# Performance work log

Hardware: AMD Instinct MI355X
Metric: run time of the kernel (lower is better)

The kernel has to match this reference:

```python
import jax, jax.numpy as jnp
import numpy as np
import math

B, S, D_MODEL = 2, 2048, 1024
H = 16
DK = D_MODEL // H          # 64, down-proj per-stream dim
NOPE, ROPE = 128, 64
D_HEAD = NOPE + ROPE       # 192 = d_latent // H
D_LATENT = H * D_HEAD      # 3072
ROT_DIM = 2 * ((ROPE // 2) // 2)  # rotary dim actually rotated = qk_rope_dim//2 = 32
EPS = 1e-6


def _rmsnorm(x, w):
    out = x * jax.lax.rsqrt(jnp.mean(x * x, axis=-1, keepdims=True) + EPS)
    return out * w


def _apply_rope(x):
    # x: [b, h, s, d]; rotate first ROT_DIM channels, interleaved pairing
    s = x.shape[-2]
    inv_freq = 1.0 / (10000.0 ** (jnp.arange(0, ROT_DIM, 2, dtype=jnp.float32) / ROT_DIM))
    freqs = jnp.arange(s, dtype=jnp.float32)[:, None] * inv_freq[None, :]  # [s, ROT_DIM//2]
    freqs = jnp.repeat(freqs, 2, axis=-1)  # [s, ROT_DIM], (f0,f0,f1,f1,...)
    cos, sin = jnp.cos(freqs), jnp.sin(freqs)
    xl, xr = x[..., :ROT_DIM], x[..., ROT_DIM:]
    x1, x2 = xl[..., 0::2], xl[..., 1::2]
    rot = jnp.stack([-x2, x1], axis=-1).reshape(xl.shape)
    xl = xl * cos + rot * sin
    return jnp.concatenate([xl, xr], axis=-1)


def setup_inputs() -> dict:
    key = jax.random.key(0)
    ks = jax.random.split(key, 5)
    sc = 0.02
    x = jax.random.normal(ks[0], (B, S, D_MODEL), jnp.float32)
    mask = jnp.broadcast_to(jnp.tril(jnp.ones((S, S), jnp.int32)), (B, S, S))
    w_down = jax.random.normal(ks[1], (D_MODEL, 3 * DK), jnp.float32) * sc
    rms_w = jnp.ones((3 * DK,), jnp.float32)
    w_up = jax.random.normal(ks[2], (3 * DK, 3 * D_LATENT), jnp.float32) * sc
    w_o = jax.random.normal(ks[3], (D_LATENT, D_MODEL), jnp.float32) * sc
    return {"x": x, "mask": mask, "w_down": w_down, "rms_w": rms_w, "w_up": w_up, "w_o": w_o}


def reference(x, mask, w_down, rms_w, w_up, w_o):
    h = x @ w_down                        # [b, s, 3*dk]
    h = _rmsnorm(h, rms_w)
    qkv = h @ w_up                        # [b, s, 3*d_latent]
    q, k, v = jnp.split(qkv, 3, axis=-1)  # each [b, s, d_latent]

    def to_heads(t):
        # einops '(d h)': d outer, h inner
        return t.reshape(B, S, D_HEAD, H).transpose(0, 3, 1, 2)  # [b, h, s, d]

    q, k, v = to_heads(q), to_heads(k), to_heads(v)
    q_nope, q_rope = q[..., :NOPE], q[..., NOPE:]
    k_nope, k_rope = k[..., :NOPE], k[..., NOPE:]
    q_rope = _apply_rope(q_rope)
    k_rope = _apply_rope(k_rope)

    scores = (jnp.einsum('bhid,bhjd->bhij', q_nope, k_nope)
              + jnp.einsum('bhid,bhjd->bhij', q_rope, k_rope))
    scores = scores / math.sqrt(NOPE + ROPE)
    scores = jnp.where(mask[:, None] == 0, -1e9, scores)
    attn = jax.nn.softmax(scores, axis=-1)

    out = jnp.einsum('bhij,bhjd->bhid', attn, v)        # [b, h, s, d]
    out = out.transpose(0, 2, 1, 3).reshape(B, S, D_LATENT)  # 'b h s d -> b s (h d)'
    return out @ w_o
```

## Files before the change

### kernel.cpp

```cpp
#include <hip/hip_runtime.h>
#include <stdint.h>
#include <stddef.h>


typedef __bf16 bf16x8 __attribute__((ext_vector_type(8)));
typedef float  f32x4  __attribute__((ext_vector_type(4)));

#define MFMA16x16(a,b,c) __builtin_amdgcn_mfma_f32_16x16x32_bf16((a),(b),(c),0,0,0)

__device__ __forceinline__ uint16_t f2bf(float f){
  union { float f; uint32_t u; } v; v.f = f;
  uint32_t u = v.u + 0x7fffu + ((v.u >> 16) & 1u);
  return (uint16_t)(u >> 16);
}
__device__ __forceinline__ bf16x8 load_frag(const uint16_t* p){
  uint4 u = *reinterpret_cast<const uint4*>(p);
  return __builtin_bit_cast(bf16x8, u);
}
__device__ __forceinline__ f32x4 fzero(){
  f32x4 z = {0.f, 0.f, 0.f, 0.f};
  return z;
}
__device__ __forceinline__ uint32_t pack2(float a, float b){
  return (uint32_t)f2bf(a) | ((uint32_t)f2bf(b) << 16);
}
__device__ __forceinline__ void gl2lds16(const uint16_t* g, uint16_t* l){
  __builtin_amdgcn_global_load_lds(
      (const __attribute__((address_space(1))) uint32_t*)g,
      (__attribute__((address_space(3))) uint32_t*)l,
      16, 0, 0);
}

__global__ __launch_bounds__(256) void k_transpose_cvt(const float* __restrict__ in,
                                                       uint16_t* __restrict__ out,
                                                       int R, int C){
  __shared__ float t[32][33];
  const int tc = blockIdx.x * 32;
  const int tr = blockIdx.y * 32;
  const int j = threadIdx.x & 31, i0 = threadIdx.x >> 5;
  for(int ii = 0; ii < 4; ++ii){
    int r = i0 + ii * 8;
    t[r][j] = in[(size_t)(tr + r) * C + tc + j];
  }
  __syncthreads();
  for(int ii = 0; ii < 4; ++ii){
    int c = i0 + ii * 8;
    out[(size_t)(tc + c) * R + tr + j] = f2bf(t[j][c]);
  }
}

__global__ __launch_bounds__(256) void k_down_mfma(const float* __restrict__ x,
                                                   const uint16_t* __restrict__ wdt,
                                                   const float* __restrict__ rms_w,
                                                   uint16_t* __restrict__ h_out){
  __shared__ __align__(16) uint16_t as[32 * 64];
  __shared__ float hsq[32];
  const int tid  = threadIdx.x;
  const int wave = tid >> 6, lane = tid & 63;
  const int ml = lane & 15, qd = lane >> 4;
  const int m0 = blockIdx.x * 32;
  const int n0w = wave * 48;
  if(tid < 32) hsq[tid] = 0.f;

  f32x4 acc[2][3];
#pragma unroll
  for(int mt = 0; mt < 2; ++mt)
#pragma unroll
    for(int nt = 0; nt < 3; ++nt) acc[mt][nt] = fzero();

  const int srow = tid >> 3, sc = tid & 7;
  for(int kt = 0; kt < 16; ++kt){
    const float* src = x + (size_t)(m0 + srow) * 1024 + kt * 64 + sc * 8;
    float4 a = *reinterpret_cast<const float4*>(src);
    float4 b = *reinterpret_cast<const float4*>(src + 4);
    uint4 pk;
    pk.x = pack2(a.x, a.y); pk.y = pack2(a.z, a.w);
    pk.z = pack2(b.x, b.y); pk.w = pack2(b.z, b.w);
    __syncthreads();
    *reinterpret_cast<uint4*>(as + srow * 64 + ((sc ^ (srow & 7)) * 8)) = pk;
    __syncthreads();
#pragma unroll
    for(int kk = 0; kk < 2; ++kk){
      bf16x8 af[2];
#pragma unroll
      for(int mt = 0; mt < 2; ++mt){
        int row = mt * 16 + ml;
        af[mt] = load_frag(as + row * 64 + (((kk * 4 + qd) ^ (row & 7)) * 8));
      }
#pragma unroll
      for(int nt = 0; nt < 3; ++nt){
        bf16x8 bfr = load_frag(wdt + (size_t)(n0w + nt * 16 + ml) * 1024 + kt * 64 + kk * 32 + qd * 8);
#pragma unroll
        for(int mt = 0; mt < 2; ++mt)
          acc[mt][nt] = MFMA16x16(af[mt], bfr, acc[mt][nt]);
      }
    }
  }
  __syncthreads();
#pragma unroll
  for(int mt = 0; mt < 2; ++mt)
#pragma unroll
    for(int r = 0; r < 4; ++r){
      float s = acc[mt][0][r]*acc[mt][0][r] + acc[mt][1][r]*acc[mt][1][r] + acc[mt][2][r]*acc[mt][2][r];
#pragma unroll
      for(int off = 1; off < 16; off <<= 1) s += __shfl_xor(s, off);
      if(ml == 0) atomicAdd(&hsq[mt * 16 + qd * 4 + r], s);
    }
  __syncthreads();
  float rw[3];
#pragma unroll
  for(int nt = 0; nt < 3; ++nt) rw[nt] = rms_w[n0w + nt * 16 + ml];
#pragma unroll
  for(int mt = 0; mt < 2; ++mt)
#pragma unroll
    for(int r = 0; r < 4; ++r){
      int row = mt * 16 + qd * 4 + r;
      float scl = rsqrtf(hsq[row] * (1.0f / 192.0f) + 1e-6f);
#pragma unroll
      for(int nt = 0; nt < 3; ++nt)
        h_out[(size_t)(m0 + row) * 192 + n0w + nt * 16 + ml] = f2bf(acc[mt][nt][r] * scl * rw[nt]);
    }
}

__global__ __launch_bounds__(256) void k_gemm_up(const uint16_t* __restrict__ hmat,
                                                 const uint16_t* __restrict__ wt,
                                                 uint16_t* __restrict__ q_t,
                                                 uint16_t* __restrict__ k_t,
                                                 uint16_t* __restrict__ v_t){
  const int wave = threadIdx.x >> 6, lane = threadIdx.x & 63;
  const int ml = lane & 15, qd = lane >> 4;
  const int m0 = blockIdx.y * 32;
  const int n0 = blockIdx.x * 256 + wave * 64;
  const int which = n0 / 3072;
  const int d0 = (n0 % 3072) >> 4;
  bf16x8 af[2][6];
#pragma unroll
  for(int mt = 0; mt < 2; ++mt)
#pragma unroll
    for(int kk = 0; kk < 6; ++kk)
      af[mt][kk] = load_frag(hmat + (size_t)(m0 + mt * 16 + ml) * 192 + kk * 32 + qd * 8);
  f32x4 acc[4][2];
#pragma unroll
  for(int nt = 0; nt < 4; ++nt){ acc[nt][0] = fzero(); acc[nt][1] = fzero(); }
#pragma unroll
  for(int nt = 0; nt < 4; ++nt){
#pragma unroll
    for(int kk = 0; kk < 6; ++kk){
      bf16x8 b = load_frag(wt + (size_t)(n0 + nt * 16 + ml) * 192 + kk * 32 + qd * 8);
      acc[nt][0] = MFMA16x16(af[0][kk], b, acc[nt][0]);
      acc[nt][1] = MFMA16x16(af[1][kk], b, acc[nt][1]);
    }
  }
  if(which < 2){
    uint16_t* dst = which ? k_t : q_t;
    const float qs = which ? 1.0f : 0.07216878364870322f;
    const int c = d0 >> 3, sub = d0 & 7;
#pragma unroll
    for(int mt = 0; mt < 2; ++mt)
#pragma unroll
      for(int r = 0; r < 4; ++r){
        int tok = m0 + mt * 16 + qd * 4 + r;
        int b = tok >> 11, s = tok & 2047;
        float v0 = acc[0][mt][r], v1 = acc[1][mt][r];
        float v2 = acc[2][mt][r], v3 = acc[3][mt][r];
        if(d0 >= 128 && d0 < 160){
#pragma unroll
          for(int p = 0; p < 2; ++p){
            int fi = (d0 + 2 * p - 128) >> 1;
            float invf = __expf(-(float)fi * 0.5756462732485114f);
            float sn, cs;
            sincosf((float)s * invf, &sn, &cs);
            float e = p ? v2 : v0, o = p ? v3 : v1;
            float ne = e * cs - o * sn, no = o * cs + e * sn;
            if(p){ v2 = ne; v3 = no; } else { v0 = ne; v1 = no; }
          }
        }
        int kt2 = s >> 6, row = s & 63;
        uint2 pk; pk.x = pack2(v0 * qs, v1 * qs); pk.y = pack2(v2 * qs, v3 * qs);
        size_t off = ((size_t)(b * 16 + ml) * 32 + kt2) * (64 * 192)
                   + row * 192 + ((c ^ (row & 7)) * 8) + sub;
        *reinterpret_cast<uint2*>(dst + off) = pk;
      }
  } else {
#pragma unroll
    for(int mt = 0; mt < 2; ++mt){
      int tok0 = m0 + mt * 16 + qd * 4;
      int b = tok0 >> 11, s0 = tok0 & 2047;
      int kt2 = s0 >> 6, col = s0 & 63;
      int cc = col >> 3, sub = col & 7;
#pragma unroll
      for(int nt = 0; nt < 4; ++nt){
        int d = d0 + nt;
        uint2 pk;
        pk.x = pack2(acc[nt][mt][0], acc[nt][mt][1]);
        pk.y = pack2(acc[nt][mt][2], acc[nt][mt][3]);
        size_t off = ((size_t)(b * 16 + ml) * 32 + kt2) * (192 * 64)
                   + d * 64 + ((cc ^ (d & 7)) * 8) + sub;
        *reinterpret_cast<uint2*>(v_t + off) = pk;
      }
    }
  }
}

__global__ __launch_bounds__(256, 3) void k_attn(const uint16_t* __restrict__ q_t,
                                                 const uint16_t* __restrict__ k_t,
                                                 const uint16_t* __restrict__ v_t,
                                                 uint16_t* __restrict__ attn_out){
  __shared__ __align__(16) uint16_t ks[64 * 192];
  __shared__ __align__(16) uint16_t vs[208 * 64];
  const int tid  = threadIdx.x;
  const int wave = tid >> 6;
  const int lane = tid & 63;
  const int ml   = lane & 15;
  const int qd   = lane >> 4;
  const int L    = blockIdx.x;
  const int idx  = L >> 3;
  const int qt   = 31 - (idx & 31);
  const int bh   = (L & 7) + ((idx >> 5) << 3);

  {
    uint32_t* vw = (uint32_t*)vs;
    vw[6144 + tid] = 0x3F803F80u;
    vw[6400 + tid] = 0x3F803F80u;
  }

  {
    const uint16_t* qtile = q_t + ((size_t)bh * 32 + qt) * (64 * 192);
#pragma unroll
    for(int it = 0; it < 6; ++it){
      int seg = it * 4 + wave;
      gl2lds16(qtile + seg * 512 + lane * 8, ks + seg * 512);
    }
  }
  __syncthreads();
  bf16x8 qf[6];
  {
    int row = wave * 16 + ml;
#pragma unroll
    for(int kk = 0; kk < 6; ++kk)
      qf[kk] = load_frag(ks + row * 192 + (((kk * 4 + qd) ^ (row & 7)) * 8));
  }

  f32x4 o[13];
#pragma unroll
  for(int i = 0; i < 13; ++i) o[i] = fzero();

  for(int kt = 0; kt <= qt; ++kt){
    __syncthreads();
    const uint16_t* ktile = k_t + ((size_t)bh * 32 + kt) * (64 * 192);
    const uint16_t* vtile = v_t + ((size_t)bh * 32 + kt) * (192 * 64);
#pragma unroll
    for(int it = 0; it < 6; ++it){
      int seg = it * 4 + wave;
      gl2lds16(ktile + seg * 512 + lane * 8, ks + seg * 512);
    }
#pragma unroll
    for(int it = 0; it < 6; ++it){
      int seg = it * 4 + wave;
      gl2lds16(vtile + seg * 512 + lane * 8, vs + seg * 512);
    }
    __syncthreads();

    float p[4][4];
    const bool diag = (kt == qt);
#pragma unroll
    for(int nt = 0; nt < 4; ++nt){
      f32x4 a = fzero();
      int row = nt * 16 + ml;
#pragma unroll
      for(int kk = 0; kk < 6; ++kk){
        bf16x8 b = load_frag(ks + row * 192 + (((kk * 4 + qd) ^ (row & 7)) * 8));
        a = MFMA16x16(qf[kk], b, a);
      }
#pragma unroll
      for(int r = 0; r < 4; ++r){
        float v = a[r];
        if(diag){
          int i = qt * 64 + wave * 16 + qd * 4 + r;
          int j = kt * 64 + nt * 16 + ml;
          if(j > i) v = -1e9f;
        }
        p[nt][r] = __expf(v);
      }
    }

    __syncthreads();
    uint16_t* psw = ks + wave * 1024;
#pragma unroll
    for(int nt = 0; nt < 4; ++nt)
#pragma unroll
      for(int r = 0; r < 4; ++r){
        int rp = qd * 4 + r;
        int col = nt * 16 + ml;
        int c = (col >> 3) ^ (rp & 7);
        psw[rp * 64 + c * 8 + (col & 7)] = f2bf(p[nt][r]);
      }
#pragma unroll
    for(int kk2 = 0; kk2 < 2; ++kk2){
      int cp = (kk2 * 4 + qd) ^ (ml & 7);
      bf16x8 pa = load_frag(psw + ml * 64 + cp * 8);
#pragma unroll
      for(int dt = 0; dt < 13; ++dt){
        int row = dt * 16 + ml;
        int cv = (kk2 * 4 + qd) ^ (row & 7);
        bf16x8 vb = load_frag(vs + row * 64 + cv * 8);
        o[dt] = MFMA16x16(pa, vb, o[dt]);
      }
    }
  }

  const int hh = bh & 15, b = bh >> 4;
#pragma unroll
  for(int r = 0; r < 4; ++r){
    int i = qt * 64 + wave * 16 + qd * 4 + r;
    float inv = 1.0f / o[12][r];
    size_t obase = ((size_t)b * 2048 + i) * 3072 + hh * 192;
#pragma unroll
    for(int dt = 0; dt < 12; ++dt)
      attn_out[obase + dt * 16 + ml] = f2bf(o[dt][r] * inv);
  }
}

__global__ __launch_bounds__(256) void k_gemm_o_tile(const uint16_t* __restrict__ a,
                                                     const uint16_t* __restrict__ wt,
                                                     float* __restrict__ part){
  __shared__ __align__(16) uint16_t as[128 * 64];
  __shared__ __align__(16) uint16_t bs[128 * 64];
  const int wave = threadIdx.x >> 6, lane = threadIdx.x & 63;
  const int ml = lane & 15, qd = lane >> 4;
  const int m0 = blockIdx.y * 128, n0 = blockIdx.x * 128;
  const int kz = blockIdx.z;
  const int mo = (wave >> 1) * 64, no = (wave & 1) * 64;

  const int lrow = lane >> 3;
  const int gch  = (lane & 7) ^ (lrow & 7);
  const uint16_t* abase = a  + (size_t)(m0 + lrow) * 3072 + kz * 1536 + gch * 8;
  const uint16_t* bbase = wt + (size_t)(n0 + lrow) * 3072 + kz * 1536 + gch * 8;

  f32x4 acc[4][4];
#pragma unroll
  for(int mt = 0; mt < 4; ++mt)
#pragma unroll
    for(int nt = 0; nt < 4; ++nt) acc[mt][nt] = fzero();

  for(int kt = 0; kt < 24; ++kt){
    __syncthreads();
#pragma unroll
    for(int it = 0; it < 4; ++it){
      int seg = it * 4 + wave;
      gl2lds16(abase + (size_t)seg * 24576 + kt * 64, as + seg * 512);
      gl2lds16(bbase + (size_t)seg * 24576 + kt * 64, bs + seg * 512);
    }
    __syncthreads();
#pragma unroll
    for(int ks2 = 0; ks2 < 2; ++ks2){
      bf16x8 af[4], bfr[4];
#pragma unroll
      for(int mt = 0; mt < 4; ++mt){
        int row = mo + mt * 16 + ml;
        af[mt] = load_frag(as + row * 64 + (((ks2 * 4 + qd) ^ (row & 7)) * 8));
      }
#pragma unroll
      for(int nt = 0; nt < 4; ++nt){
        int row = no + nt * 16 + ml;
        bfr[nt] = load_frag(bs + row * 64 + (((ks2 * 4 + qd) ^ (row & 7)) * 8));
      }
#pragma unroll
      for(int mt = 0; mt < 4; ++mt)
#pragma unroll
        for(int nt = 0; nt < 4; ++nt)
          acc[mt][nt] = MFMA16x16(af[mt], bfr[nt], acc[mt][nt]);
    }
  }

  float* dst = part + (size_t)kz * 4096 * 1024;
#pragma unroll
  for(int mt = 0; mt < 4; ++mt)
#pragma unroll
    for(int nt = 0; nt < 4; ++nt)
#pragma unroll
      for(int r = 0; r < 4; ++r){
        int row = m0 + mo + mt * 16 + qd * 4 + r;
        int col = n0 + no + nt * 16 + ml;
        dst[(size_t)row * 1024 + col] = acc[mt][nt][r];
      }
}

__global__ __launch_bounds__(256) void k_addout(const float* __restrict__ part,
                                                float* __restrict__ out){
  int i = blockIdx.x * 256 + threadIdx.x;
  const float4* p0 = (const float4*)part;
  const float4* p1 = p0 + (size_t)1048576;
  float4 a = p0[i], b = p1[i];
  float4 c; c.x = a.x + b.x; c.y = a.y + b.y; c.z = a.z + b.z; c.w = a.w + b.w;
  ((float4*)out)[i] = c;
}


extern "C" void kernel_launch(void* const* d_in, const int* in_sizes, int n_in,
                              void* d_out, int out_size, void* d_ws, size_t ws_size,
                              hipStream_t stream) {
  (void)in_sizes; (void)n_in; (void)out_size; (void)ws_size;
  const float* x      = (const float*)d_in[0];
  const float* w_down = (const float*)d_in[2];
  const float* rms_w  = (const float*)d_in[3];
  const float* w_up   = (const float*)d_in[4];
  const float* w_o    = (const float*)d_in[5];
  float* out = (float*)d_out;

  char* ws = (char*)d_ws;
  uint16_t* h_bf   = (uint16_t*)(ws);
  uint16_t* w_up_t = (uint16_t*)(ws + 1572864);
  uint16_t* w_o_t  = (uint16_t*)(ws + 5111808);
  uint16_t* w_dn_t = (uint16_t*)(ws + 11403264);
  uint16_t* q_tb   = (uint16_t*)(ws + 11796480);
  uint16_t* k_tb   = (uint16_t*)(ws + 36962304);
  uint16_t* v_tb   = (uint16_t*)(ws + 62128128);
  uint16_t* attnO  = (uint16_t*)(ws + 87293952);
  float*    part   = (float*)(ws + 11796480);

  k_transpose_cvt<<<dim3(288, 6), 256, 0, stream>>>(w_up, w_up_t, 192, 9216);
  k_transpose_cvt<<<dim3(32, 96), 256, 0, stream>>>(w_o,  w_o_t,  3072, 1024);
  k_transpose_cvt<<<dim3(6, 32),  256, 0, stream>>>(w_down, w_dn_t, 1024, 192);
  k_down_mfma<<<128, 256, 0, stream>>>(x, w_dn_t, rms_w, h_bf);
  k_gemm_up<<<dim3(36, 128), 256, 0, stream>>>(h_bf, w_up_t, q_tb, k_tb, v_tb);
  k_attn<<<1024, 256, 0, stream>>>(q_tb, k_tb, v_tb, attnO);
  k_gemm_o_tile<<<dim3(8, 32, 2), 256, 0, stream>>>(attnO, w_o_t, part);
  k_addout<<<4096, 256, 0, stream>>>(part, out);
}
```

Measured before the change: 375.9 us.

## Stage up-projection output through LDS for coalesced 16-byte Q/K/V stores

```diff
diff --git a/kernel.cpp b/kernel.cpp
--- a/kernel.cpp
+++ b/kernel.cpp
@@ -127,77 +127,111 @@
                                                  uint16_t* __restrict__ q_t,
                                                  uint16_t* __restrict__ k_t,
                                                  uint16_t* __restrict__ v_t){
+  __shared__ __align__(16) uint16_t rp[16 * 129 * 8];
   const int wave = threadIdx.x >> 6, lane = threadIdx.x & 63;
   const int ml = lane & 15, qd = lane >> 4;
   const int m0 = blockIdx.y * 32;
-  const int n0 = blockIdx.x * 256 + wave * 64;
-  const int which = n0 / 3072;
-  const int d0 = (n0 % 3072) >> 4;
+  const int bx = blockIdx.x;
+  const int which = bx / 6;
+  const int d0b = (bx % 6) * 32;
+  const int n0w = bx * 512 + wave * 128;
+  const int d0w = d0b + wave * 8;
+
   bf16x8 af[2][6];
 #pragma unroll
   for(int mt = 0; mt < 2; ++mt)
 #pragma unroll
     for(int kk = 0; kk < 6; ++kk)
       af[mt][kk] = load_frag(hmat + (size_t)(m0 + mt * 16 + ml) * 192 + kk * 32 + qd * 8);
-  f32x4 acc[4][2];
-#pragma unroll
-  for(int nt = 0; nt < 4; ++nt){ acc[nt][0] = fzero(); acc[nt][1] = fzero(); }
-#pragma unroll
-  for(int nt = 0; nt < 4; ++nt){
+
+  f32x4 acc[8][2];
+#pragma unroll
+  for(int nt = 0; nt < 8; ++nt){ acc[nt][0] = fzero(); acc[nt][1] = fzero(); }
+#pragma unroll
+  for(int nt = 0; nt < 8; ++nt){
 #pragma unroll
     for(int kk = 0; kk < 6; ++kk){
-      bf16x8 b = load_frag(wt + (size_t)(n0 + nt * 16 + ml) * 192 + kk * 32 + qd * 8);
+      bf16x8 b = load_frag(wt + (size_t)(n0w + nt * 16 + ml) * 192 + kk * 32 + qd * 8);
       acc[nt][0] = MFMA16x16(af[0][kk], b, acc[nt][0]);
       acc[nt][1] = MFMA16x16(af[1][kk], b, acc[nt][1]);
     }
   }
+
+  const int b   = m0 >> 11;
+  const int s0  = m0 & 2047;
+  const int kt2 = s0 >> 6;
+  const int row0 = s0 & 63;
+  uint4* rp4 = (uint4*)rp;
+
   if(which < 2){
-    uint16_t* dst = which ? k_t : q_t;
     const float qs = which ? 1.0f : 0.07216878364870322f;
-    const int c = d0 >> 3, sub = d0 & 7;
+    const bool rope = (d0w >= 128) && (d0w < 160);
 #pragma unroll
     for(int mt = 0; mt < 2; ++mt)
 #pragma unroll
       for(int r = 0; r < 4; ++r){
-        int tok = m0 + mt * 16 + qd * 4 + r;
-        int b = tok >> 11, s = tok & 2047;
-        float v0 = acc[0][mt][r], v1 = acc[1][mt][r];
-        float v2 = acc[2][mt][r], v3 = acc[3][mt][r];
-        if(d0 >= 128 && d0 < 160){
-#pragma unroll
-          for(int p = 0; p < 2; ++p){
-            int fi = (d0 + 2 * p - 128) >> 1;
+        int t = mt * 16 + qd * 4 + r;
+        int s = s0 + t;
+        float v[8];
+#pragma unroll
+        for(int nt = 0; nt < 8; ++nt) v[nt] = acc[nt][mt][r] * qs;
+        if(rope){
+#pragma unroll
+          for(int pi = 0; pi < 4; ++pi){
+            int fi = (d0w + 2 * pi - 128) >> 1;
             float invf = __expf(-(float)fi * 0.5756462732485114f);
             float sn, cs;
             sincosf((float)s * invf, &sn, &cs);
-            float e = p ? v2 : v0, o = p ? v3 : v1;
-            float ne = e * cs - o * sn, no = o * cs + e * sn;
-            if(p){ v2 = ne; v3 = no; } else { v0 = ne; v1 = no; }
+            float e = v[2 * pi], o = v[2 * pi + 1];
+            v[2 * pi]     = e * cs - o * sn;
+            v[2 * pi + 1] = o * cs + e * sn;
           }
         }
-        int kt2 = s >> 6, row = s & 63;
-        uint2 pk; pk.x = pack2(v0 * qs, v1 * qs); pk.y = pack2(v2 * qs, v3 * qs);
-        size_t off = ((size_t)(b * 16 + ml) * 32 + kt2) * (64 * 192)
-                   + row * 192 + ((c ^ (row & 7)) * 8) + sub;
-        *reinterpret_cast<uint2*>(dst + off) = pk;
+        uint4 pk;
+        pk.x = pack2(v[0], v[1]); pk.y = pack2(v[2], v[3]);
+        pk.z = pack2(v[4], v[5]); pk.w = pack2(v[6], v[7]);
+        rp4[ml * 129 + t * 4 + (wave ^ (t & 3))] = pk;
       }
   } else {
 #pragma unroll
-    for(int mt = 0; mt < 2; ++mt){
-      int tok0 = m0 + mt * 16 + qd * 4;
-      int b = tok0 >> 11, s0 = tok0 & 2047;
-      int kt2 = s0 >> 6, col = s0 & 63;
-      int cc = col >> 3, sub = col & 7;
-#pragma unroll
-      for(int nt = 0; nt < 4; ++nt){
-        int d = d0 + nt;
+    for(int nt = 0; nt < 8; ++nt){
+      int dl = wave * 8 + nt;
+#pragma unroll
+      for(int mt = 0; mt < 2; ++mt){
+        int jc = mt * 2 + (qd >> 1);
+        int slot = ml * 129 + dl * 4 + (jc ^ (dl & 3));
         uint2 pk;
         pk.x = pack2(acc[nt][mt][0], acc[nt][mt][1]);
         pk.y = pack2(acc[nt][mt][2], acc[nt][mt][3]);
-        size_t off = ((size_t)(b * 16 + ml) * 32 + kt2) * (192 * 64)
-                   + d * 64 + ((cc ^ (d & 7)) * 8) + sub;
-        *reinterpret_cast<uint2*>(v_t + off) = pk;
-      }
+        *(reinterpret_cast<uint2*>(rp + slot * 8) + (qd & 1)) = pk;
+      }
+    }
+  }
+  __syncthreads();
+
+  if(which < 2){
+    uint16_t* dst = which ? k_t : q_t;
+    const int cb = d0b >> 3;
+#pragma unroll
+    for(int it = 0; it < 8; ++it){
+      int h = wave * 4 + (it & 3), rhalf = it >> 2;
+      int tloc = rhalf * 16 + (lane >> 2), p = lane & 3;
+      int row = row0 + tloc;
+      uint4 val = rp4[h * 129 + tloc * 4 + p];
+      size_t off = ((size_t)(b * 16 + h) * 32 + kt2) * 12288
+                 + (size_t)row * 192 + ((cb ^ (tloc & 4)) + p) * 8;
+      *reinterpret_cast<uint4*>(dst + off) = val;
+    }
+  } else {
+    const int cs0 = row0 >> 3;
+#pragma unroll
+    for(int it = 0; it < 8; ++it){
+      int h = wave * 4 + (it & 3), dhalf = it >> 2;
+      int dl = dhalf * 16 + (lane >> 2), p = lane & 3;
+      uint4 val = rp4[h * 129 + dl * 4 + p];
+      size_t off = ((size_t)(b * 16 + h) * 32 + kt2) * 12288
+                 + (size_t)(d0b + dl) * 64 + ((cs0 ^ (dl & 4)) + p) * 8;
+      *reinterpret_cast<uint4*>(v_t + off) = val;
     }
   }
 }
@@ -290,10 +324,10 @@
     for(int nt = 0; nt < 4; ++nt)
 #pragma unroll
       for(int r = 0; r < 4; ++r){
-        int rp = qd * 4 + r;
+        int rp2 = qd * 4 + r;
         int col = nt * 16 + ml;
-        int c = (col >> 3) ^ (rp & 7);
-        psw[rp * 64 + c * 8 + (col & 7)] = f2bf(p[nt][r]);
+        int c = (col >> 3) ^ (rp2 & 7);
+        psw[rp2 * 64 + c * 8 + (col & 7)] = f2bf(p[nt][r]);
       }
 #pragma unroll
     for(int kk2 = 0; kk2 < 2; ++kk2){
@@ -423,7 +457,7 @@
   k_transpose_cvt<<<dim3(32, 96), 256, 0, stream>>>(w_o,  w_o_t,  3072, 1024);
   k_transpose_cvt<<<dim3(6, 32),  256, 0, stream>>>(w_down, w_dn_t, 1024, 192);
   k_down_mfma<<<128, 256, 0, stream>>>(x, w_dn_t, rms_w, h_bf);
-  k_gemm_up<<<dim3(36, 128), 256, 0, stream>>>(h_bf, w_up_t, q_tb, k_tb, v_tb);
+  k_gemm_up<<<dim3(18, 128), 256, 0, stream>>>(h_bf, w_up_t, q_tb, k_tb, v_tb);
   k_attn<<<1024, 256, 0, stream>>>(q_tb, k_tb, v_tb, attnO);
   k_gemm_o_tile<<<dim3(8, 32, 2), 256, 0, stream>>>(attnO, w_o_t, part);
   k_addout<<<4096, 256, 0, stream>>>(part, out);
```

New measurement: 354.4 us. 5.7% less time.
